# Kernel optimization log

Measured on AMD Instinct MI355X. Metric: run time of the kernel, lower is better.

## Reference

```python
import jax, jax.numpy as jnp
import numpy as np
import math

HIDDEN = 1024
HEADS = 16
D_K = HIDDEN // HEADS
EPS = 1e-5


def gelu_tanh(x):
    c = math.sqrt(2.0 / math.pi)
    return 0.5 * x * (1.0 + jnp.tanh(c * (x + 0.044715 * x ** 3)))


def layer_norm(x, gamma, beta):
    mu = jnp.mean(x, axis=-1, keepdims=True)
    var = jnp.mean((x - mu) ** 2, axis=-1, keepdims=True)
    return (x - mu) * jax.lax.rsqrt(var + EPS) * gamma + beta


def setup_inputs() -> dict:
    key = jax.random.key(0)
    ks = jax.random.split(key, 12)
    s = 1.0 / math.sqrt(HIDDEN)
    s4 = 1.0 / math.sqrt(4 * HIDDEN)
    inp = {
        "x": jax.random.normal(ks[0], (2, 2048, HIDDEN), dtype=jnp.float32),
        # attention linears, stored as (in, out) so y = x @ W + b
        "Wq": jax.random.uniform(ks[1], (HIDDEN, HIDDEN), minval=-s, maxval=s),
        "bq": jax.random.uniform(ks[2], (HIDDEN,), minval=-s, maxval=s),
        "Wv": jax.random.uniform(ks[3], (HIDDEN, HIDDEN), minval=-s, maxval=s),
        "bv": jax.random.uniform(ks[4], (HIDDEN,), minval=-s, maxval=s),
        "Wo": jax.random.uniform(ks[5], (HIDDEN, HIDDEN), minval=-s, maxval=s),
        "bo": jax.random.uniform(ks[6], (HIDDEN,), minval=-s, maxval=s),
        # feed-forward
        "W1": jax.random.uniform(ks[7], (HIDDEN, 4 * HIDDEN), minval=-s, maxval=s),
        "b1": jax.random.uniform(ks[8], (4 * HIDDEN,), minval=-s, maxval=s),
        "W2": jax.random.uniform(ks[9], (4 * HIDDEN, HIDDEN), minval=-s4, maxval=s4),
        "b2": jax.random.uniform(ks[10], (HIDDEN,), minval=-s4, maxval=s4),
        # layer norms
        "g1": jnp.ones((HIDDEN,), jnp.float32),
        "beta1": jnp.zeros((HIDDEN,), jnp.float32),
        "g2": jnp.ones((HIDDEN,), jnp.float32),
        "beta2": jnp.zeros((HIDDEN,), jnp.float32),
    }
    return inp


def attention(x, Wq, bq, Wv, bv, Wo, bo):
    bs, seq, _ = x.shape
    qk = (x @ Wq + bq).reshape(bs, seq, HEADS, D_K).transpose(0, 2, 1, 3)  # b h s d
    v = (x @ Wv + bv).reshape(bs, seq, HEADS, D_K).transpose(0, 2, 1, 3)
    scores = jnp.einsum('bhqd,bhkd->bhqk', qk, qk) / math.sqrt(D_K)
    causal = jnp.tril(jnp.ones((seq, seq), dtype=bool))
    scores = jnp.where(causal[None, None], scores, -jnp.inf)
    attn = jax.nn.softmax(scores, axis=-1)
    out = jnp.einsum('bhqk,bhkd->bhqd', attn, v)
    out = out.transpose(0, 2, 1, 3).reshape(bs, seq, HIDDEN)
    return out @ Wo + bo


def reference(x, Wq, bq, Wv, bv, Wo, bo, W1, b1, W2, b2, g1, beta1, g2, beta2):
    x = x + attention(layer_norm(x, g1, beta1), Wq, bq, Wv, bv, Wo, bo)
    h = layer_norm(x, g2, beta2)
    ff = gelu_tanh(h @ W1 + b1) @ W2 + b2  # chunking is a memory detail; same math
    return x + ff
```

## Files before the change

kernel.cpp:

```cpp
#include <hip/hip_runtime.h>

typedef unsigned short u16;
typedef short bf16x8 __attribute__((ext_vector_type(8)));
typedef float f32x4 __attribute__((ext_vector_type(4)));

__device__ __forceinline__ float bf2f(u16 u) {
    union { unsigned int i; float f; } v; v.i = ((unsigned int)u) << 16; return v.f;
}
__device__ __forceinline__ u16 f2bf(float f) {
    union { float f; unsigned int i; } v; v.f = f;
    unsigned int r = v.i + 0x7fffu + ((v.i >> 16) & 1u);
    return (u16)(r >> 16);
}

__device__ __forceinline__ void gload16(const u16* g, u16* l) {
    __builtin_amdgcn_global_load_lds((__attribute__((address_space(1))) void*)(u16*)g,
                                     (__attribute__((address_space(3))) void*)l, 16, 0, 0);
}

__global__ __launch_bounds__(256) void prep(const float* __restrict__ Wq,
                                            const float* __restrict__ Wv,
                                            const float* __restrict__ Wo,
                                            const float* __restrict__ W1,
                                            const float* __restrict__ W2,
                                            const float* __restrict__ bq,
                                            const float* __restrict__ bv,
                                            const float* __restrict__ x,
                                            const float* __restrict__ g1,
                                            const float* __restrict__ be1,
                                            u16* __restrict__ WqT, u16* __restrict__ WvT,
                                            u16* __restrict__ WoT, u16* __restrict__ W1T,
                                            u16* __restrict__ W2T, float* __restrict__ bqv,
                                            u16* __restrict__ h1) {
    int id = blockIdx.x;
    int tid = threadIdx.x;
    if (id >= 2824) {
        int row = id - 2824;
        int lane = tid & 63, wave = tid >> 6;
        float4 f4 = *(const float4*)(x + (size_t)row * 1024 + tid * 4);
        float v[4] = {f4.x, f4.y, f4.z, f4.w};
        float s1 = v[0] + v[1] + v[2] + v[3];
        float s2 = v[0]*v[0] + v[1]*v[1] + v[2]*v[2] + v[3]*v[3];
#pragma unroll
        for (int mm = 1; mm < 64; mm <<= 1) { s1 += __shfl_xor(s1, mm); s2 += __shfl_xor(s2, mm); }
        __shared__ float a1[4], a2[4];
        if (lane == 0) { a1[wave] = s1; a2[wave] = s2; }
        __syncthreads();
        s1 = a1[0] + a1[1] + a1[2] + a1[3];
        s2 = a2[0] + a2[1] + a2[2] + a2[3];
        float mean = s1 * (1.0f / 1024.0f);
        float var  = s2 * (1.0f / 1024.0f) - mean * mean;
        float rstd = rsqrtf(var + 1e-5f);
#pragma unroll
        for (int i = 0; i < 4; ++i) {
            int c = tid * 4 + i;
            h1[(size_t)row * 1024 + c] = f2bf((v[i] - mean) * rstd * g1[c] + be1[c]);
        }
        return;
    }
    if (id >= 2816) {
        int i = (id - 2816) * 256 + tid;
        bqv[i] = (i < 1024) ? bq[i] : bv[i - 1024];
        return;
    }
    const float* in; u16* out; int R, C, bx, by;
    if (id < 256)       { in = Wq; out = WqT; R = 1024; C = 1024; bx = id & 15;          by = id >> 4; }
    else if (id < 512)  { int t = id - 256;  in = Wv; out = WvT; R = 1024; C = 1024; bx = t & 15; by = t >> 4; }
    else if (id < 768)  { int t = id - 512;  in = Wo; out = WoT; R = 1024; C = 1024; bx = t & 15; by = t >> 4; }
    else if (id < 1792) { int t = id - 768;  in = W1; out = W1T; R = 1024; C = 4096; bx = t & 63; by = t >> 6; }
    else                { int t = id - 1792; in = W2; out = W2T; R = 4096; C = 1024; bx = t & 15; by = t >> 4; }
    __shared__ u16 tile[64][65];
    int c0 = bx * 64, r0 = by * 64;
    for (int i = tid; i < 4096; i += 256) {
        int r = i >> 6, c = i & 63;
        tile[r][c] = f2bf(in[(size_t)(r0 + r) * C + c0 + c]);
    }
    __syncthreads();
    for (int i = tid; i < 4096; i += 256) {
        int r = i >> 6, c = i & 63;
        out[(size_t)(c0 + r) * R + r0 + c] = tile[c][r];
    }
}

__global__ __launch_bounds__(256) void transpose_bf16_s(const u16* __restrict__ in,
                                                        u16* __restrict__ out,
                                                        int R, int C, int istride) {
    __shared__ u16 tile[64][65];
    int c0 = blockIdx.x * 64, r0 = blockIdx.y * 64;
    in  += (size_t)blockIdx.z * R * istride;
    out += (size_t)blockIdx.z * R * C;
    for (int i = threadIdx.x; i < 4096; i += 256) {
        int r = i >> 6, c = i & 63;
        tile[r][c] = in[(size_t)(r0 + r) * istride + c0 + c];
    }
    __syncthreads();
    for (int i = threadIdx.x; i < 4096; i += 256) {
        int r = i >> 6, c = i & 63;
        out[(size_t)(c0 + r) * R + r0 + c] = tile[c][r];
    }
}

__global__ __launch_bounds__(256) void ln_bf16(const u16* __restrict__ x,
                                               const float* __restrict__ g,
                                               const float* __restrict__ be,
                                               u16* __restrict__ out) {
    int row = blockIdx.x, tid = threadIdx.x;
    int lane = tid & 63, wave = tid >> 6;
    u16 e[4]; *(uint2*)e = *(const uint2*)(x + (size_t)row * 1024 + tid * 4);
    float v[4];
#pragma unroll
    for (int i = 0; i < 4; ++i) v[i] = bf2f(e[i]);
    float s1 = v[0] + v[1] + v[2] + v[3];
    float s2 = v[0]*v[0] + v[1]*v[1] + v[2]*v[2] + v[3]*v[3];
#pragma unroll
    for (int mm = 1; mm < 64; mm <<= 1) { s1 += __shfl_xor(s1, mm); s2 += __shfl_xor(s2, mm); }
    __shared__ float a1[4], a2[4];
    if (lane == 0) { a1[wave] = s1; a2[wave] = s2; }
    __syncthreads();
    s1 = a1[0] + a1[1] + a1[2] + a1[3];
    s2 = a2[0] + a2[1] + a2[2] + a2[3];
    float mean = s1 * (1.0f / 1024.0f);
    float var  = s2 * (1.0f / 1024.0f) - mean * mean;
    float rstd = rsqrtf(var + 1e-5f);
#pragma unroll
    for (int i = 0; i < 4; ++i) {
        int c = tid * 4 + i;
        out[(size_t)row * 1024 + c] = f2bf((v[i] - mean) * rstd * g[c] + be[c]);
    }
}

template <int BN, int ACT, int RES, typename OutT>
__global__ __launch_bounds__(256) void gemm_gl(const u16* __restrict__ A,
                                               const u16* __restrict__ WT,
                                               const float* __restrict__ bias,
                                               const float* __restrict__ resid,
                                               OutT* __restrict__ C,
                                               int M, int N, int K, int cpx) {
    constexpr int JN = BN / 32;
    __shared__ u16 lds_a[128 * 64];
    __shared__ u16 lds_b[BN * 64];
    int tid = threadIdx.x;
    int lane = tid & 63, wave = tid >> 6;
    int l16 = lane & 15, quad = lane >> 4;
    int wm = (wave >> 1) * 64, wn = (wave & 1) * (BN / 2);

    int id = blockIdx.x;
    int slot = id >> 3;
    int bx = (id & 7) * cpx + (slot >> 5);
    int by = slot & 31;
    int m0 = by * 128, n0 = bx * BN;
    f32x4 acc[4][JN] = {};

    int scol = ((lane & 7) ^ (lane >> 3)) * 8;
    const u16* Ab = A  + (size_t)(m0 + wave * 8 + (lane >> 3)) * K + scol;
    const u16* Bb = WT + (size_t)(n0 + wave * 8 + (lane >> 3)) * K + scol;
    u16* la = lds_a + wave * 512;
    u16* lb = lds_b + wave * 512;
    int xk = (l16 & 7);

    for (int k0 = 0; k0 < K; k0 += 64) {
        __syncthreads();
#pragma unroll
        for (int it = 0; it < 4; ++it)
            gload16(Ab + (size_t)it * 32 * K + k0, la + it * 2048);
#pragma unroll
        for (int it = 0; it < JN; ++it)
            gload16(Bb + (size_t)it * 32 * K + k0, lb + it * 2048);
        __syncthreads();
#pragma unroll
        for (int s = 0; s < 2; ++s) {
            bf16x8 af[4], bfr[JN];
#pragma unroll
            for (int i = 0; i < 4; ++i)
                af[i] = *(const bf16x8*)&lds_a[(wm + i * 16 + l16) * 64 + (((s * 4 + quad) ^ xk) * 8)];
#pragma unroll
            for (int j = 0; j < JN; ++j)
                bfr[j] = *(const bf16x8*)&lds_b[(wn + j * 16 + l16) * 64 + (((s * 4 + quad) ^ xk) * 8)];
#pragma unroll
            for (int i = 0; i < 4; ++i)
#pragma unroll
                for (int j = 0; j < JN; ++j)
                    acc[i][j] = __builtin_amdgcn_mfma_f32_16x16x32_bf16(af[i], bfr[j], acc[i][j], 0, 0, 0);
        }
    }

#pragma unroll
    for (int j = 0; j < JN; ++j) {
        int col = n0 + wn + j * 16 + l16;
        float bv = bias[col];
#pragma unroll
        for (int i = 0; i < 4; ++i) {
            int rbase = m0 + wm + i * 16 + quad * 4;
#pragma unroll
            for (int r = 0; r < 4; ++r) {
                size_t idx = (size_t)(rbase + r) * N + col;
                float v = acc[i][j][r] + bv;
                if (ACT == 1) {
                    float u = v;
                    float y = 0.7978845608028654f * (u + 0.044715f * u * u * u);
                    float t = __expf(2.0f * y);
                    float th = 1.0f - 2.0f / (t + 1.0f);
                    v = 0.5f * u * (1.0f + th);
                }
                if (RES) v += resid[idx];
                if constexpr (sizeof(OutT) == 4) C[idx] = v;
                else                             C[idx] = f2bf(v);
            }
        }
    }
}

template <int ACT>
__global__ __launch_bounds__(256, 2) void gemm_big(const u16* __restrict__ A,
                                                   const u16* __restrict__ WT,
                                                   const float* __restrict__ bias,
                                                   u16* __restrict__ C,
                                                   int M, int N, int K) {
    __shared__ u16 lds_a[256 * 64];
    __shared__ u16 lds_b[128 * 64];
    int tid = threadIdx.x;
    int lane = tid & 63, wave = tid >> 6;
    int l16 = lane & 15, quad = lane >> 4;
    int wm = (wave >> 1) * 128, wn = (wave & 1) * 64;
    int id = blockIdx.x;
    int bx = id & 31, by = id >> 5;
    int m0 = by * 256, n0 = bx * 128;
    f32x4 acc[8][4] = {};

    int scol = ((lane & 7) ^ (lane >> 3)) * 8;
    const u16* Ab = A  + (size_t)(m0 + wave * 8 + (lane >> 3)) * K + scol;
    const u16* Bb = WT + (size_t)(n0 + wave * 8 + (lane >> 3)) * K + scol;
    u16* la = lds_a + wave * 512;
    u16* lb = lds_b + wave * 512;
    int xk = (l16 & 7);

    for (int k0 = 0; k0 < K; k0 += 64) {
        __syncthreads();
#pragma unroll
        for (int it = 0; it < 8; ++it)
            gload16(Ab + (size_t)it * 32 * K + k0, la + it * 2048);
#pragma unroll
        for (int it = 0; it < 4; ++it)
            gload16(Bb + (size_t)it * 32 * K + k0, lb + it * 2048);
        __syncthreads();
#pragma unroll
        for (int s = 0; s < 2; ++s) {
            bf16x8 bfr[4];
#pragma unroll
            for (int j = 0; j < 4; ++j)
                bfr[j] = *(const bf16x8*)&lds_b[(wn + j * 16 + l16) * 64 + (((s * 4 + quad) ^ xk) * 8)];
#pragma unroll
            for (int i = 0; i < 8; ++i) {
                bf16x8 af = *(const bf16x8*)&lds_a[(wm + i * 16 + l16) * 64 + (((s * 4 + quad) ^ xk) * 8)];
#pragma unroll
                for (int j = 0; j < 4; ++j)
                    acc[i][j] = __builtin_amdgcn_mfma_f32_16x16x32_bf16(af, bfr[j], acc[i][j], 0, 0, 0);
            }
        }
    }

#pragma unroll
    for (int j = 0; j < 4; ++j) {
        int col = n0 + wn + j * 16 + l16;
        float bv = bias[col];
#pragma unroll
        for (int i = 0; i < 8; ++i) {
            int rbase = m0 + wm + i * 16 + quad * 4;
#pragma unroll
            for (int r = 0; r < 4; ++r) {
                size_t idx = (size_t)(rbase + r) * N + col;
                float v = acc[i][j][r] + bv;
                if (ACT == 1) {
                    float u = v;
                    float y = 0.7978845608028654f * (u + 0.044715f * u * u * u);
                    float t = __expf(2.0f * y);
                    float th = 1.0f - 2.0f / (t + 1.0f);
                    v = 0.5f * u * (1.0f + th);
                }
                C[idx] = f2bf(v);
            }
        }
    }
}

__global__ __launch_bounds__(256, 2) void gemm_split(const u16* __restrict__ A,
                                                     const u16* __restrict__ WT,
                                                     u16* __restrict__ p0,
                                                     u16* __restrict__ p1,
                                                     u16* __restrict__ p2,
                                                     int M, int N, int K) {
    __shared__ u16 lds_a[256 * 64];
    __shared__ u16 lds_b[128 * 64];
    int tid = threadIdx.x;
    int lane = tid & 63, wave = tid >> 6;
    int l16 = lane & 15, quad = lane >> 4;
    int wm = (wave >> 1) * 128, wn = (wave & 1) * 64;
    int id = blockIdx.x;
    int slice = id >> 7;
    int t = id & 127;
    int bx = t & 7, by = t >> 3;
    int m0 = by * 256, n0 = bx * 128;
    int k_lo = (slice == 0) ? 0 : 64 * (22 + 21 * (slice - 1));
    int k_hi = (slice == 2) ? K : 64 * (22 + 21 * slice);
    u16* P = (slice == 0) ? p0 : (slice == 1) ? p1 : p2;
    f32x4 acc[8][4] = {};

    int scol = ((lane & 7) ^ (lane >> 3)) * 8;
    const u16* Ab = A  + (size_t)(m0 + wave * 8 + (lane >> 3)) * K + scol;
    const u16* Bb = WT + (size_t)(n0 + wave * 8 + (lane >> 3)) * K + scol;
    u16* la = lds_a + wave * 512;
    u16* lb = lds_b + wave * 512;
    int xk = (l16 & 7);

    for (int k0 = k_lo; k0 < k_hi; k0 += 64) {
        __syncthreads();
#pragma unroll
        for (int it = 0; it < 8; ++it)
            gload16(Ab + (size_t)it * 32 * K + k0, la + it * 2048);
#pragma unroll
        for (int it = 0; it < 4; ++it)
            gload16(Bb + (size_t)it * 32 * K + k0, lb + it * 2048);
        __syncthreads();
#pragma unroll
        for (int s = 0; s < 2; ++s) {
            bf16x8 bfr[4];
#pragma unroll
            for (int j = 0; j < 4; ++j)
                bfr[j] = *(const bf16x8*)&lds_b[(wn + j * 16 + l16) * 64 + (((s * 4 + quad) ^ xk) * 8)];
#pragma unroll
            for (int i = 0; i < 8; ++i) {
                bf16x8 af = *(const bf16x8*)&lds_a[(wm + i * 16 + l16) * 64 + (((s * 4 + quad) ^ xk) * 8)];
#pragma unroll
                for (int j = 0; j < 4; ++j)
                    acc[i][j] = __builtin_amdgcn_mfma_f32_16x16x32_bf16(af, bfr[j], acc[i][j], 0, 0, 0);
            }
        }
    }

#pragma unroll
    for (int j = 0; j < 4; ++j) {
        int col = n0 + wn + j * 16 + l16;
#pragma unroll
        for (int i = 0; i < 8; ++i) {
            int rbase = m0 + wm + i * 16 + quad * 4;
#pragma unroll
            for (int r = 0; r < 4; ++r)
                P[(size_t)(rbase + r) * N + col] = f2bf(acc[i][j][r]);
        }
    }
}

__global__ __launch_bounds__(256) void ff2_reduce(const u16* __restrict__ p0,
                                                  const u16* __restrict__ p1,
                                                  const u16* __restrict__ p2,
                                                  const u16* __restrict__ x2b,
                                                  const float* __restrict__ b2,
                                                  float* __restrict__ out) {
    size_t i = ((size_t)blockIdx.x * 256 + threadIdx.x) * 8;
    int col = (int)(i & 1023);
    uint4 a0 = *(const uint4*)&p0[i];
    uint4 a1 = *(const uint4*)&p1[i];
    uint4 a2 = *(const uint4*)&p2[i];
    uint4 ax = *(const uint4*)&x2b[i];
    const u16* e0 = (const u16*)&a0;
    const u16* e1 = (const u16*)&a1;
    const u16* e2 = (const u16*)&a2;
    const u16* ex = (const u16*)&ax;
    float o[8];
#pragma unroll
    for (int e = 0; e < 8; ++e)
        o[e] = bf2f(ex[e]) + bf2f(e0[e]) + bf2f(e1[e]) + bf2f(e2[e]) + b2[col + e];
    *(float4*)&out[i]     = *(float4*)&o[0];
    *(float4*)&out[i + 4] = *(float4*)&o[4];
}

__global__ __launch_bounds__(256) void attn_kernel(const u16* __restrict__ QV,
                                                   const u16* __restrict__ Vt,
                                                   u16* __restrict__ Out) {
    int id = blockIdx.x;
    int slot = id >> 3;
    int hb = (id & 7) + 8 * (slot & 3);
    int t  = 31 - (slot >> 2);
    int h = hb & 15, b = hb >> 4;
    int tid = threadIdx.x;
    int lane = tid & 63, wave = tid >> 6;
    int l16 = lane & 15, quad = lane >> 4;

    __shared__ u16 k_lds[64 * 64];
    __shared__ u16 v_lds[64 * 64];
    __shared__ u16 p_lds[4][16 * 72];

    bf16x8 ones;
#pragma unroll
    for (int e = 0; e < 8; ++e) ones[e] = (short)0x3F80;

    int srow = wave * 8 + (lane >> 3);
    int sc8  = ((lane & 7) ^ (lane >> 3)) * 8;
    int xk   = (l16 & 7);

    int q0 = t * 64;
    const u16* qp = QV + ((size_t)b * 2048 + q0 + wave * 16 + l16) * 2048 + h * 64;
    bf16x8 qf[2];
    qf[0] = *(const bf16x8*)&qp[quad * 8];
    qf[1] = *(const bf16x8*)&qp[32 + quad * 8];

    f32x4 O[4] = {};
    f32x4 L = {};

    for (int kt = 0; kt <= t; ++kt) {
        const u16* kg = QV + ((size_t)b * 2048 + kt * 64 + srow) * 2048 + h * 64 + sc8;
        const u16* vg = Vt + ((((size_t)b * 16 + h) * 64) + srow) * 2048 + kt * 64 + sc8;
        __syncthreads();
        gload16(kg,                      k_lds + wave * 512);
        gload16(kg + (size_t)32 * 2048,  k_lds + wave * 512 + 2048);
        gload16(vg,                      v_lds + wave * 512);
        gload16(vg + (size_t)32 * 2048,  v_lds + wave * 512 + 2048);
        __syncthreads();

        f32x4 S[4] = {};
#pragma unroll
        for (int s = 0; s < 2; ++s)
#pragma unroll
            for (int j = 0; j < 4; ++j) {
                bf16x8 kf = *(const bf16x8*)&k_lds[(j * 16 + l16) * 64 + (((s * 4 + quad) ^ xk) * 8)];
                S[j] = __builtin_amdgcn_mfma_f32_16x16x32_bf16(qf[s], kf, S[j], 0, 0, 0);
            }

        if (kt == t) {
#pragma unroll
            for (int j = 0; j < 4; ++j) {
                int key = j * 16 + l16;
#pragma unroll
                for (int r = 0; r < 4; ++r)
                    if (key > wave * 16 + quad * 4 + r) S[j][r] = -1e30f;
            }
        }

#pragma unroll
        for (int j = 0; j < 4; ++j)
#pragma unroll
            for (int r = 0; r < 4; ++r) {
                float pp = __expf(S[j][r] * 0.125f);
                p_lds[wave][(quad * 4 + r) * 72 + j * 16 + l16] = f2bf(pp);
            }

#pragma unroll
        for (int s = 0; s < 2; ++s) {
            bf16x8 pf = *(const bf16x8*)&p_lds[wave][l16 * 72 + s * 32 + quad * 8];
            L = __builtin_amdgcn_mfma_f32_16x16x32_bf16(pf, ones, L, 0, 0, 0);
#pragma unroll
            for (int dj = 0; dj < 4; ++dj) {
                bf16x8 vf = *(const bf16x8*)&v_lds[(dj * 16 + l16) * 64 + (((s * 4 + quad) ^ xk) * 8)];
                O[dj] = __builtin_amdgcn_mfma_f32_16x16x32_bf16(pf, vf, O[dj], 0, 0, 0);
            }
        }
    }

#pragma unroll
    for (int r = 0; r < 4; ++r) {
        int qg = q0 + wave * 16 + quad * 4 + r;
        float inv = 1.0f / L[r];
#pragma unroll
        for (int dj = 0; dj < 4; ++dj)
            Out[((size_t)b * 2048 + qg) * 1024 + h * 64 + dj * 16 + l16] =
                f2bf(O[dj][r] * inv);
    }
}

extern "C" void kernel_launch(void* const* d_in, const int* in_sizes, int n_in,
                              void* d_out, int out_size, void* d_ws, size_t ws_size,
                              hipStream_t stream) {
    const float* x   = (const float*)d_in[0];
    const float* Wq  = (const float*)d_in[1];
    const float* bq  = (const float*)d_in[2];
    const float* Wv  = (const float*)d_in[3];
    const float* bv  = (const float*)d_in[4];
    const float* Wo  = (const float*)d_in[5];
    const float* bo  = (const float*)d_in[6];
    const float* W1  = (const float*)d_in[7];
    const float* b1  = (const float*)d_in[8];
    const float* W2  = (const float*)d_in[9];
    const float* b2  = (const float*)d_in[10];
    const float* g1  = (const float*)d_in[11];
    const float* be1 = (const float*)d_in[12];
    const float* g2  = (const float*)d_in[13];
    const float* be2 = (const float*)d_in[14];

    char* ws = (char*)d_ws;
    const size_t MB = 1 << 20;
    u16*   WqT  = (u16*)(ws + 0  * MB);
    u16*   WvT  = (u16*)(ws + 2  * MB);
    u16*   WoT  = (u16*)(ws + 4  * MB);
    u16*   W1T  = (u16*)(ws + 6  * MB);
    u16*   W2T  = (u16*)(ws + 14 * MB);
    u16*   h1   = (u16*)(ws + 22 * MB);
    u16*   QV   = (u16*)(ws + 30 * MB);
    u16*   x2b  = (u16*)(ws + 30 * MB);
    u16*   Vt   = (u16*)(ws + 46 * MB);
    u16*   ff1  = (u16*)(ws + 46 * MB);
    float* bqv  = (float*)(ws + 78 * MB);
    u16*   fp0  = (u16*)(ws + 0  * MB);
    u16*   fp1  = (u16*)(ws + 22 * MB);
    u16*   fp2  = (u16*)(ws + 38 * MB);

    prep<<<6920, 256, 0, stream>>>(Wq, Wv, Wo, W1, W2, bq, bv, x, g1, be1,
                                   WqT, WvT, WoT, W1T, W2T, bqv, h1);

    gemm_gl<128, 0, 0, u16><<<512, 256, 0, stream>>>(h1, WqT, bqv, nullptr, QV, 4096, 2048, 1024, 2);

    transpose_bf16_s<<<dim3(16, 32, 2), 256, 0, stream>>>(QV + 1024, Vt, 2048, 1024, 2048);

    attn_kernel<<<1024, 256, 0, stream>>>(QV, Vt, h1);

    gemm_gl<64, 0, 1, u16><<<512, 256, 0, stream>>>(h1, WoT, bo, x, x2b, 4096, 1024, 1024, 2);

    ln_bf16<<<4096, 256, 0, stream>>>(x2b, g2, be2, h1);

    gemm_big<1><<<512, 256, 0, stream>>>(h1, W1T, b1, ff1, 4096, 4096, 1024);

    gemm_split<<<384, 256, 0, stream>>>(ff1, W2T, fp0, fp1, fp2, 4096, 1024, 4096);

    ff2_reduce<<<2048, 256, 0, stream>>>(fp0, fp1, fp2, x2b, b2, (float*)d_out);
}
```

Before: 319.0 us.

## Fuse V transpose into QV GEMM epilogue and stage GEMM stores through LDS

The Q/V projection GEMM now writes Q to a compact 1024-wide buffer and writes V directly in the transposed per-head layout the attention kernel needs. This removes the separate transpose kernel and its extra read and write of V. Every GEMM epilogue (gemm_gl, gemm_big, gemm_split) now stages bf16 results in LDS and writes 16-byte coalesced rows, replacing scattered 2-byte stores. The cost is extra __syncthreads per row group in the epilogue, and the V blocks make uint2 stores strided by sequence length.

```diff
diff --git a/kernel.cpp b/kernel.cpp
--- a/kernel.cpp
+++ b/kernel.cpp
@@ -11,6 +11,11 @@
     union { float f; unsigned int i; } v; v.f = f;
     unsigned int r = v.i + 0x7fffu + ((v.i >> 16) & 1u);
     return (u16)(r >> 16);
+}
+__device__ __forceinline__ float gelu(float u) {
+    float y = 0.7978845608028654f * (u + 0.044715f * u * u * u);
+    float t = __expf(2.0f * y);
+    return 0.5f * u * (1.0f + (1.0f - 2.0f / (t + 1.0f)));
 }
 
 __device__ __forceinline__ void gload16(const u16* g, u16* l) {
@@ -82,24 +87,6 @@
     }
 }
 
-__global__ __launch_bounds__(256) void transpose_bf16_s(const u16* __restrict__ in,
-                                                        u16* __restrict__ out,
-                                                        int R, int C, int istride) {
-    __shared__ u16 tile[64][65];
-    int c0 = blockIdx.x * 64, r0 = blockIdx.y * 64;
-    in  += (size_t)blockIdx.z * R * istride;
-    out += (size_t)blockIdx.z * R * C;
-    for (int i = threadIdx.x; i < 4096; i += 256) {
-        int r = i >> 6, c = i & 63;
-        tile[r][c] = in[(size_t)(r0 + r) * istride + c0 + c];
-    }
-    __syncthreads();
-    for (int i = threadIdx.x; i < 4096; i += 256) {
-        int r = i >> 6, c = i & 63;
-        out[(size_t)(c0 + r) * R + r0 + c] = tile[c][r];
-    }
-}
-
 __global__ __launch_bounds__(256) void ln_bf16(const u16* __restrict__ x,
                                                const float* __restrict__ g,
                                                const float* __restrict__ be,
@@ -129,14 +116,16 @@
     }
 }
 
-template <int BN, int ACT, int RES, typename OutT>
+template <int BN, int ACT, int RES, int VSPLIT>
 __global__ __launch_bounds__(256) void gemm_gl(const u16* __restrict__ A,
                                                const u16* __restrict__ WT,
                                                const float* __restrict__ bias,
                                                const float* __restrict__ resid,
-                                               OutT* __restrict__ C,
+                                               u16* __restrict__ C,
+                                               u16* __restrict__ Vt,
                                                int M, int N, int K, int cpx) {
     constexpr int JN = BN / 32;
+    constexpr int TS = BN + 8;
     __shared__ u16 lds_a[128 * 64];
     __shared__ u16 lds_b[BN * 64];
     int tid = threadIdx.x;
@@ -184,28 +173,58 @@
         }
     }
 
-#pragma unroll
-    for (int j = 0; j < JN; ++j) {
-        int col = n0 + wn + j * 16 + l16;
-        float bv = bias[col];
-#pragma unroll
-        for (int i = 0; i < 4; ++i) {
-            int rbase = m0 + wm + i * 16 + quad * 4;
+    if (VSPLIT && n0 >= 1024) {
+        int b = m0 >> 11;
+#pragma unroll
+        for (int j = 0; j < JN; ++j) {
+            int col = n0 + wn + j * 16 + l16;
+            float bv = bias[col];
+            int hh = (col >> 6) & 15;
+            int d  = col & 63;
+#pragma unroll
+            for (int i = 0; i < 4; ++i) {
+                int sb = (m0 & 2047) + wm + i * 16 + quad * 4;
+                u16 pk[4];
+#pragma unroll
+                for (int r = 0; r < 4; ++r) pk[r] = f2bf(acc[i][j][r] + bv);
+                *(uint2*)&Vt[((((size_t)b * 16 + hh) * 64) + d) * 2048 + sb] = *(uint2*)pk;
+            }
+        }
+        return;
+    }
+
+    u16* et = lds_a;
+    int erow = tid >> 3;
+    int lr0  = (wave >> 1) * 16 + quad * 4;
+    float bvj[JN];
+#pragma unroll
+    for (int j = 0; j < JN; ++j) bvj[j] = bias[n0 + wn + j * 16 + l16];
+#pragma unroll
+    for (int i = 0; i < 4; ++i) {
+        __syncthreads();
+#pragma unroll
+        for (int j = 0; j < JN; ++j) {
+            int col = wn + j * 16 + l16;
 #pragma unroll
             for (int r = 0; r < 4; ++r) {
-                size_t idx = (size_t)(rbase + r) * N + col;
-                float v = acc[i][j][r] + bv;
-                if (ACT == 1) {
-                    float u = v;
-                    float y = 0.7978845608028654f * (u + 0.044715f * u * u * u);
-                    float t = __expf(2.0f * y);
-                    float th = 1.0f - 2.0f / (t + 1.0f);
-                    v = 0.5f * u * (1.0f + th);
-                }
-                if (RES) v += resid[idx];
-                if constexpr (sizeof(OutT) == 4) C[idx] = v;
-                else                             C[idx] = f2bf(v);
-            }
+                float v = acc[i][j][r] + bvj[j];
+                if (ACT) v = gelu(v);
+                if (RES) v += resid[(size_t)(m0 + wm + i * 16 + quad * 4 + r) * N + n0 + col];
+                et[(lr0 + r) * TS + col] = f2bf(v);
+            }
+        }
+        __syncthreads();
+        int grow = m0 + (erow >> 4) * 64 + i * 16 + (erow & 15);
+        if (BN == 128) {
+            int ec = (tid & 7) * 16;
+            uint4 d0 = *(const uint4*)&et[erow * TS + ec];
+            uint4 d1 = *(const uint4*)&et[erow * TS + ec + 8];
+            *(uint4*)&C[(size_t)grow * N + n0 + ec]     = d0;
+            *(uint4*)&C[(size_t)grow * N + n0 + ec + 8] = d1;
+        } else {
+            int ec = (tid & 7) * 8;
+            uint4 d0 = *(const uint4*)&et[erow * TS + ec];
+            *(uint4*)&C[(size_t)grow * N + n0 + ec] = d0;
         }
     }
 }
@@ -259,27 +278,33 @@
         }
     }
 
-#pragma unroll
-    for (int j = 0; j < 4; ++j) {
-        int col = n0 + wn + j * 16 + l16;
-        float bv = bias[col];
-#pragma unroll
-        for (int i = 0; i < 8; ++i) {
-            int rbase = m0 + wm + i * 16 + quad * 4;
+    constexpr int TS = 136;
+    u16* et = lds_a;
+    int erow = tid >> 3;
+    int ec   = (tid & 7) * 16;
+    int lr0  = (wave >> 1) * 16 + quad * 4;
+    float bvj[4];
+#pragma unroll
+    for (int j = 0; j < 4; ++j) bvj[j] = bias[n0 + wn + j * 16 + l16];
+#pragma unroll
+    for (int i = 0; i < 8; ++i) {
+        __syncthreads();
+#pragma unroll
+        for (int j = 0; j < 4; ++j) {
+            int col = wn + j * 16 + l16;
 #pragma unroll
             for (int r = 0; r < 4; ++r) {
-                size_t idx = (size_t)(rbase + r) * N + col;
-                float v = acc[i][j][r] + bv;
-                if (ACT == 1) {
-                    float u = v;
-                    float y = 0.7978845608028654f * (u + 0.044715f * u * u * u);
-                    float t = __expf(2.0f * y);
-                    float th = 1.0f - 2.0f / (t + 1.0f);
-                    v = 0.5f * u * (1.0f + th);
-                }
-                C[idx] = f2bf(v);
-            }
-        }
+                float v = acc[i][j][r] + bvj[j];
+                if (ACT) v = gelu(v);
+                et[(lr0 + r) * TS + col] = f2bf(v);
+            }
+        }
+        __syncthreads();
+        int grow = m0 + (erow >> 4) * 128 + i * 16 + (erow & 15);
+        uint4 d0 = *(const uint4*)&et[erow * TS + ec];
+        uint4 d1 = *(const uint4*)&et[erow * TS + ec + 8];
+        *(uint4*)&C[(size_t)grow * N + n0 + ec]     = d0;
+        *(uint4*)&C[(size_t)grow * N + n0 + ec + 8] = d1;
     }
 }
 
@@ -337,16 +362,27 @@
         }
     }
 
-#pragma unroll
-    for (int j = 0; j < 4; ++j) {
-        int col = n0 + wn + j * 16 + l16;
-#pragma unroll
-        for (int i = 0; i < 8; ++i) {
-            int rbase = m0 + wm + i * 16 + quad * 4;
+    constexpr int TS = 136;
+    u16* et = lds_a;
+    int erow = tid >> 3;
+    int ec   = (tid & 7) * 16;
+    int lr0  = (wave >> 1) * 16 + quad * 4;
+#pragma unroll
+    for (int i = 0; i < 8; ++i) {
+        __syncthreads();
+#pragma unroll
+        for (int j = 0; j < 4; ++j) {
+            int col = wn + j * 16 + l16;
 #pragma unroll
             for (int r = 0; r < 4; ++r)
-                P[(size_t)(rbase + r) * N + col] = f2bf(acc[i][j][r]);
-        }
+                et[(lr0 + r) * TS + col] = f2bf(acc[i][j][r]);
+        }
+        __syncthreads();
+        int grow = m0 + (erow >> 4) * 128 + i * 16 + (erow & 15);
+        uint4 d0 = *(const uint4*)&et[erow * TS + ec];
+        uint4 d1 = *(const uint4*)&et[erow * TS + ec + 8];
+        *(uint4*)&P[(size_t)grow * N + n0 + ec]     = d0;
+        *(uint4*)&P[(size_t)grow * N + n0 + ec + 8] = d1;
     }
 }
 
@@ -374,7 +410,7 @@
     *(float4*)&out[i + 4] = *(float4*)&o[4];
 }
 
-__global__ __launch_bounds__(256) void attn_kernel(const u16* __restrict__ QV,
+__global__ __launch_bounds__(256) void attn_kernel(const u16* __restrict__ Qb,
                                                    const u16* __restrict__ Vt,
                                                    u16* __restrict__ Out) {
     int id = blockIdx.x;
@@ -399,7 +435,7 @@
     int xk   = (l16 & 7);
 
     int q0 = t * 64;
-    const u16* qp = QV + ((size_t)b * 2048 + q0 + wave * 16 + l16) * 2048 + h * 64;
+    const u16* qp = Qb + ((size_t)b * 2048 + q0 + wave * 16 + l16) * 1024 + h * 64;
     bf16x8 qf[2];
     qf[0] = *(const bf16x8*)&qp[quad * 8];
     qf[1] = *(const bf16x8*)&qp[32 + quad * 8];
@@ -408,11 +444,11 @@
     f32x4 L = {};
 
     for (int kt = 0; kt <= t; ++kt) {
-        const u16* kg = QV + ((size_t)b * 2048 + kt * 64 + srow) * 2048 + h * 64 + sc8;
+        const u16* kg = Qb + ((size_t)b * 2048 + kt * 64 + srow) * 1024 + h * 64 + sc8;
         const u16* vg = Vt + ((((size_t)b * 16 + h) * 64) + srow) * 2048 + kt * 64 + sc8;
         __syncthreads();
         gload16(kg,                      k_lds + wave * 512);
-        gload16(kg + (size_t)32 * 2048,  k_lds + wave * 512 + 2048);
+        gload16(kg + (size_t)32 * 1024,  k_lds + wave * 512 + 2048);
         gload16(vg,                      v_lds + wave * 512);
         gload16(vg + (size_t)32 * 2048,  v_lds + wave * 512 + 2048);
         __syncthreads();
@@ -494,7 +530,7 @@
     u16*   W1T  = (u16*)(ws + 6  * MB);
     u16*   W2T  = (u16*)(ws + 14 * MB);
     u16*   h1   = (u16*)(ws + 22 * MB);
-    u16*   QV   = (u16*)(ws + 30 * MB);
+    u16*   Qb   = (u16*)(ws + 30 * MB);
     u16*   x2b  = (u16*)(ws + 30 * MB);
     u16*   Vt   = (u16*)(ws + 46 * MB);
     u16*   ff1  = (u16*)(ws + 46 * MB);
@@ -506,13 +542,11 @@
     prep<<<6920, 256, 0, stream>>>(Wq, Wv, Wo, W1, W2, bq, bv, x, g1, be1,
                                    WqT, WvT, WoT, W1T, W2T, bqv, h1);
 
-    gemm_gl<128, 0, 0, u16><<<512, 256, 0, stream>>>(h1, WqT, bqv, nullptr, QV, 4096, 2048, 1024, 2);
-
-    transpose_bf16_s<<<dim3(16, 32, 2), 256, 0, stream>>>(QV + 1024, Vt, 2048, 1024, 2048);
-
-    attn_kernel<<<1024, 256, 0, stream>>>(QV, Vt, h1);
-
-    gemm_gl<64, 0, 1, u16><<<512, 256, 0, stream>>>(h1, WoT, bo, x, x2b, 4096, 1024, 1024, 2);
+    gemm_gl<128, 0, 0, 1><<<512, 256, 0, stream>>>(h1, WqT, bqv, nullptr, Qb, Vt, 4096, 1024, 1024, 2);
+
+    attn_kernel<<<1024, 256, 0, stream>>>(Qb, Vt, h1);
+
+    gemm_gl<64, 0, 1, 0><<<512, 256, 0, stream>>>(h1, WoT, bo, (const float*)x, x2b, nullptr, 4096, 1024, 1024, 2);
 
     ln_bf16<<<4096, 256, 0, stream>>>(x2b, g2, be2, h1);
 
```

New measurement: 324.2 us. About the same (+1.6%).
